# Optimization experiments

Measured on AMD Instinct MI355X. Metric: run time of the kernel, lower is better.

The kernel has to match this reference:

```python
import jax, jax.numpy as jnp
import numpy as np

# Decoder (keras) config: embed_dim=128, num_heads=8, num_att_layers=3, clip=10.0
B, NQ, NC, E, H, L, D = 512, 64, 1000, 128, 8, 3, 4
HD = E // H          # head_depth = 16
CLIP = 10.0


def setup_inputs() -> dict:
    key = jax.random.key(0)
    ks = jax.random.split(key, 12)
    s = 1.0 / np.sqrt(E)

    def w(k, shape):
        return jax.random.normal(k, shape, jnp.float32) * s

    return {
        "h": jax.random.normal(ks[0], (B, NQ, E), jnp.float32),
        "c": jax.random.normal(ks[1], (B, NC, E), jnp.float32),
        "mask": jnp.zeros((B, NQ, NC + 1), bool),
        "clusters": jnp.zeros((B, D, NC), bool),
        "depot_id": 0,
        # stacked per-layer GAT (multi-head self-attention) params [L, E, E]/[L, E]
        "gat_Wq": w(ks[2], (L, E, E)), "gat_bq": jnp.zeros((L, E), jnp.float32),
        "gat_Wk": w(ks[3], (L, E, E)), "gat_bk": jnp.zeros((L, E), jnp.float32),
        "gat_Wv": w(ks[4], (L, E, E)), "gat_bv": jnp.zeros((L, E), jnp.float32),
        "gat_Wo": w(ks[5], (L, E, E)), "gat_bo": jnp.zeros((L, E), jnp.float32),
        # decoder query/key dense layers (use_bias=True)
        "Wq": w(ks[6], (E, E)), "bq": jnp.zeros((E,), jnp.float32),
        "Wk": w(ks[7], (E, E)), "bk": jnp.zeros((E,), jnp.float32),
    }


def _mha_layer(x, Wq, bq, Wk, bk, Wv, bv, Wo, bo):
    # One Graph_Attention_Module: multi-head self-attention + residual.
    Bx, N, Ex = x.shape
    q = (x @ Wq + bq).reshape(Bx, N, H, HD)
    k = (x @ Wk + bk).reshape(Bx, N, H, HD)
    v = (x @ Wv + bv).reshape(Bx, N, H, HD)
    att = jax.nn.softmax(jnp.einsum('bqhd,bkhd->bhqk', q, k) / np.sqrt(HD), axis=-1)
    o = jnp.einsum('bhqk,bkhd->bqhd', att, v).reshape(Bx, N, Ex)
    return x + o @ Wo + bo


def reference(h, c, mask, clusters, depot_id,
              gat_Wq, gat_bq, gat_Wk, gat_bk, gat_Wv, gat_bv, gat_Wo, gat_bo,
              Wq, bq, Wk, bk):
    # --- MHGAT ---
    x = h
    for i in range(L):  # small fixed layer loop
        x = _mha_layer(x, gat_Wq[i], gat_bq[i], gat_Wk[i], gat_bk[i],
                       gat_Wv[i], gat_bv[i], gat_Wo[i], gat_bo[i])
    query = x @ Wq + bq            # [B, NQ, E]
    key = c @ Wk + bk              # [B, NC, E]
    # tanh-clipped compatibility: tanh(QK^T / sqrt(head_depth)) * clip
    compat = jnp.tanh(jnp.einsum('bqe,bke->bqk', query, key) / np.sqrt(HD)) * CLIP
    compat = jnp.where(mask[:, :, 1:], -jnp.inf, compat)   # drop depot column of mask

    # --- select_cust (vectorized: masked log_softmax + argmax per batch) ---
    compts = jnp.mean(compat, axis=1)          # [B, NC]
    clust = clusters[:, depot_id, :]           # [B, NC]
    tt = jnp.where(clust, -jnp.inf, compts)
    log_p = jax.nn.log_softmax(tt, axis=-1)
    action = jnp.argmax(log_p, axis=-1)[:, None]  # [B, 1]
    return action, compat
```

## Files before the change

### kernel.cpp

```cpp
#include <hip/hip_runtime.h>
#include <math.h>

#define NB   512
#define NQ   64
#define NCC  1000
#define EE   128
#define HH   8
#define HDD  16
#define NL   3
#define DD   4
#define CCH  64
#define XP   136
#define VP   72

typedef __bf16 bf16x8 __attribute__((ext_vector_type(8)));
typedef unsigned short u16x8 __attribute__((ext_vector_type(8)));
typedef unsigned short u16x4 __attribute__((ext_vector_type(4)));
typedef unsigned int   u32x4 __attribute__((ext_vector_type(4)));
typedef float f32x4  __attribute__((ext_vector_type(4)));
typedef float f32x16 __attribute__((ext_vector_type(16)));

__device__ __forceinline__ unsigned short f2bf(float x) {
  union { float f; unsigned u; } v; v.f = x;
  unsigned r = (v.u + 0x7fffu + ((v.u >> 16) & 1u)) >> 16;
  return (unsigned short)r;
}
__device__ __forceinline__ float bf2f(unsigned short h) {
  union { unsigned u; float f; } v; v.u = ((unsigned)h) << 16;
  return v.f;
}
__device__ __forceinline__ bf16x8 ld8(const unsigned short* p) {
  return __builtin_bit_cast(bf16x8, *(const u16x8*)p);
}
__device__ __forceinline__ float tanh10_q(float s) {
  const float e = __expf(s * 0.5f);
  return 10.f - 20.f * __builtin_amdgcn_rcpf(e + 1.f);
}
__device__ __forceinline__ int swz(int row, int cb) {
  return row * 256 + (cb ^ ((row & 7) << 4));
}

__global__ __launch_bounds__(256) void wprep_kernel(
    const float* __restrict__ gWq, const float* __restrict__ gWk,
    const float* __restrict__ gWv, const float* __restrict__ gWo,
    const float* __restrict__ Wq,  const float* __restrict__ Wk,
    unsigned short* __restrict__ gwt_hi, unsigned short* __restrict__ gwt_lo,
    unsigned short* __restrict__ wkf_hi, unsigned short* __restrict__ wkf_lo)
{
  const int idx = blockIdx.x * 256 + threadIdx.x;
  const int m = idx >> 14;
  const int r = idx & 16383;
  const int k = r >> 7, n = r & 127;
  const float* src;
  if (m < 12) {
    const int l = m >> 2, w = m & 3;
    src = (w == 0 ? gWq : w == 1 ? gWk : w == 2 ? gWv : gWo) + l * 16384;
  } else if (m == 12) src = Wq;
  else                src = Wk;
  const float v = src[k * EE + n];
  const unsigned short h  = f2bf(v);
  const unsigned short lo = f2bf(v - bf2f(h));
  if (m < 13) {
    gwt_hi[(size_t)m * 16384 + n * EE + k] = h;
    gwt_lo[(size_t)m * 16384 + n * EE + k] = lo;
  } else {
    const int nt = n >> 4, l15 = n & 15;
    const int k4 = k >> 5, qd = (k >> 3) & 3, j = k & 7;
    const int off = (((nt * 4 + k4) * 64) + qd * 16 + l15) * 8 + j;
    wkf_hi[off] = h;
    wkf_lo[off] = lo;
  }
}

__global__ __launch_bounds__(512, 1) void gat_query_mfma(
    const float* __restrict__ hin,
    const unsigned short* __restrict__ gwt_hi,
    const unsigned short* __restrict__ gwt_lo,
    const float* __restrict__ gbq, const float* __restrict__ gbk,
    const float* __restrict__ gbv, const float* __restrict__ gbo,
    const float* __restrict__ bq,
    unsigned short* __restrict__ qhi, unsigned short* __restrict__ qlo)
{
  __shared__ unsigned short XH[64 * XP], XL[64 * XP];
  __shared__ unsigned short QH[64 * XP], QL[64 * XP];
  __shared__ unsigned short KH[64 * XP], KL[64 * XP];
  __shared__ unsigned short VTH[128 * VP], VTL[128 * VP];

  const int b    = blockIdx.x;
  const int tid  = threadIdx.x;
  const int wid  = tid >> 6;
  const int lane = tid & 63;
  const int l15  = lane & 15;
  const int quad = lane >> 4;
  const int col  = lane & 31;
  const int hi32 = lane >> 5;

  for (int idx = tid; idx < NQ * EE; idx += 512) {
    const float v = hin[(size_t)b * NQ * EE + idx];
    const int r = idx >> 7, c = idx & 127;
    const unsigned short h = f2bf(v);
    XH[r * XP + c] = h;
    XL[r * XP + c] = f2bf(v - bf2f(h));
  }
  __syncthreads();

  const int mt = wid >> 1, nh = wid & 1;
  const int r0 = mt * 16;

  for (int l = 0; l < NL; ++l) {
    {
      bf16x8 axh[4], axl[4];
      #pragma unroll
      for (int k4 = 0; k4 < 4; ++k4) {
        axh[k4] = ld8(&XH[(r0 + l15) * XP + k4 * 32 + quad * 8]);
        axl[k4] = ld8(&XL[(r0 + l15) * XP + k4 * 32 + quad * 8]);
      }
      #pragma unroll
      for (int m = 0; m < 3; ++m) {
        const unsigned short* WH = gwt_hi + (size_t)(l * 4 + m) * 16384;
        const unsigned short* WL = gwt_lo + (size_t)(l * 4 + m) * 16384;
        const float* bias = (m == 0 ? gbq : (m == 1 ? gbk : gbv)) + l * EE;
        #pragma unroll
        for (int ntl = 0; ntl < 4; ++ntl) {
          const int n = (nh * 4 + ntl) * 16 + l15;
          f32x4 acc = (f32x4){0.f, 0.f, 0.f, 0.f};
          #pragma unroll
          for (int k4 = 0; k4 < 4; ++k4) {
            const int k0 = k4 * 32 + quad * 8;
            const bf16x8 bh = ld8(&WH[n * EE + k0]);
            const bf16x8 bl = ld8(&WL[n * EE + k0]);
            acc = __builtin_amdgcn_mfma_f32_16x16x32_bf16(axh[k4], bh, acc, 0, 0, 0);
            acc = __builtin_amdgcn_mfma_f32_16x16x32_bf16(axh[k4], bl, acc, 0, 0, 0);
            acc = __builtin_amdgcn_mfma_f32_16x16x32_bf16(axl[k4], bh, acc, 0, 0, 0);
          }
          const float bv = bias[n];
          if (m == 2) {
            u16x4 hv, lv;
            #pragma unroll
            for (int r = 0; r < 4; ++r) {
              const float v = acc[r] + bv;
              const unsigned short h = f2bf(v);
              hv[r] = h;
              lv[r] = f2bf(v - bf2f(h));
            }
            *(u16x4*)&VTH[n * VP + r0 + quad * 4] = hv;
            *(u16x4*)&VTL[n * VP + r0 + quad * 4] = lv;
          } else {
            unsigned short* DH = m ? KH : QH;
            unsigned short* DL = m ? KL : QL;
            #pragma unroll
            for (int r = 0; r < 4; ++r) {
              const int crow = r0 + quad * 4 + r;
              const float v = acc[r] + bv;
              const unsigned short h = f2bf(v);
              DH[crow * XP + n] = h;
              DL[crow * XP + n] = f2bf(v - bf2f(h));
            }
          }
        }
      }
    }
    __syncthreads();

    {
      const int hwid = wid;
      const int hb = hwid * 16 + hi32 * 8;
      bf16x8 akh[2], akl[2], qbh[2], qbl[2];
      #pragma unroll
      for (int t = 0; t < 2; ++t) {
        akh[t] = ld8(&KH[(t * 32 + col) * XP + hb]);
        akl[t] = ld8(&KL[(t * 32 + col) * XP + hb]);
        qbh[t] = ld8(&QH[(t * 32 + col) * XP + hb]);
        qbl[t] = ld8(&QL[(t * 32 + col) * XP + hb]);
      }

      bf16x8 pah[2][4], pal[2][4];
      #pragma unroll
      for (int qt = 0; qt < 2; ++qt) {
        f32x16 sAcc[2];
        #pragma unroll
        for (int kt = 0; kt < 2; ++kt) {
          #pragma unroll
          for (int i = 0; i < 16; ++i) sAcc[kt][i] = 0.f;
          sAcc[kt] = __builtin_amdgcn_mfma_f32_32x32x16_bf16(akh[kt], qbh[qt], sAcc[kt], 0, 0, 0);
          sAcc[kt] = __builtin_amdgcn_mfma_f32_32x32x16_bf16(akh[kt], qbl[qt], sAcc[kt], 0, 0, 0);
          sAcc[kt] = __builtin_amdgcn_mfma_f32_32x32x16_bf16(akl[kt], qbh[qt], sAcc[kt], 0, 0, 0);
        }
        float p[2][16];
        float mx = -INFINITY;
        #pragma unroll
        for (int kt = 0; kt < 2; ++kt)
          #pragma unroll
          for (int r = 0; r < 16; ++r) {
            p[kt][r] = sAcc[kt][r] * 0.25f;
            mx = fmaxf(mx, p[kt][r]);
          }
        mx = fmaxf(mx, __shfl_xor(mx, 32));
        float sum = 0.f;
        #pragma unroll
        for (int kt = 0; kt < 2; ++kt)
          #pragma unroll
          for (int r = 0; r < 16; ++r) {
            p[kt][r] = exp2f((p[kt][r] - mx) * 1.4426950408889634f);
            sum += p[kt][r];
          }
        sum += __shfl_xor(sum, 32);
        const float inv = 1.f / sum;

        unsigned pkh[2][8], pkl[2][8], swh[2][8], swl[2][8];
        #pragma unroll
        for (int kt = 0; kt < 2; ++kt)
          #pragma unroll
          for (int w = 0; w < 8; ++w) {
            const float v0 = p[kt][w * 2]     * inv;
            const float v1 = p[kt][w * 2 + 1] * inv;
            const unsigned short h0 = f2bf(v0);
            const unsigned short l0 = f2bf(v0 - bf2f(h0));
            const unsigned short h1 = f2bf(v1);
            const unsigned short l1 = f2bf(v1 - bf2f(h1));
            pkh[kt][w] = (unsigned)h0 | ((unsigned)h1 << 16);
            pkl[kt][w] = (unsigned)l0 | ((unsigned)l1 << 16);
            swh[kt][w] = (unsigned)__shfl_xor((int)pkh[kt][w], 32);
            swl[kt][w] = (unsigned)__shfl_xor((int)pkl[kt][w], 32);
          }
        const bool top = (hi32 != 0);
        #pragma unroll
        for (int ks = 0; ks < 4; ++ks) {
          const int kt = ks >> 1, hf = ks & 1;
          u32x4 wh, wl;
          wh[0] = top ? swh[kt][4 * hf + 2] : pkh[kt][4 * hf + 0];
          wh[1] = top ? swh[kt][4 * hf + 3] : pkh[kt][4 * hf + 1];
          wh[2] = top ? pkh[kt][4 * hf + 2] : swh[kt][4 * hf + 0];
          wh[3] = top ? pkh[kt][4 * hf + 3] : swh[kt][4 * hf + 1];
          wl[0] = top ? swl[kt][4 * hf + 2] : pkl[kt][4 * hf + 0];
          wl[1] = top ? swl[kt][4 * hf + 3] : pkl[kt][4 * hf + 1];
          wl[2] = top ? pkl[kt][4 * hf + 2] : swl[kt][4 * hf + 0];
          wl[3] = top ? pkl[kt][4 * hf + 3] : swl[kt][4 * hf + 1];
          pah[qt][ks] = __builtin_bit_cast(bf16x8, wh);
          pal[qt][ks] = __builtin_bit_cast(bf16x8, wl);
        }
      }

      bf16x8 bvh[4], bvl[4];
      const int vrow = hwid * 16 + (col & 15);
      #pragma unroll
      for (int ks = 0; ks < 4; ++ks) {
        bvh[ks] = ld8(&VTH[vrow * VP + ks * 16 + hi32 * 8]);
        bvl[ks] = ld8(&VTL[vrow * VP + ks * 16 + hi32 * 8]);
      }
      f32x16 accO[2];
      #pragma unroll
      for (int qt = 0; qt < 2; ++qt) {
        #pragma unroll
        for (int i = 0; i < 16; ++i) accO[qt][i] = 0.f;
        #pragma unroll
        for (int ks = 0; ks < 4; ++ks) {
          accO[qt] = __builtin_amdgcn_mfma_f32_32x32x16_bf16(pah[qt][ks], bvh[ks], accO[qt], 0, 0, 0);
          accO[qt] = __builtin_amdgcn_mfma_f32_32x32x16_bf16(pah[qt][ks], bvl[ks], accO[qt], 0, 0, 0);
          accO[qt] = __builtin_amdgcn_mfma_f32_32x32x16_bf16(pal[qt][ks], bvh[ks], accO[qt], 0, 0, 0);
        }
      }
      if (col < 16) {
        #pragma unroll
        for (int qt = 0; qt < 2; ++qt)
          #pragma unroll
          for (int r = 0; r < 16; ++r) {
            const int qrow = qt * 32 + (r & 3) + 8 * (r >> 2) + 4 * hi32;
            const float v = accO[qt][r];
            const unsigned short h = f2bf(v);
            KH[qrow * XP + hwid * 16 + col] = h;
            KL[qrow * XP + hwid * 16 + col] = f2bf(v - bf2f(h));
          }
      }
    }
    __syncthreads();

    {
      bf16x8 aoh[4], aol[4];
      #pragma unroll
      for (int k4 = 0; k4 < 4; ++k4) {
        aoh[k4] = ld8(&KH[(r0 + l15) * XP + k4 * 32 + quad * 8]);
        aol[k4] = ld8(&KL[(r0 + l15) * XP + k4 * 32 + quad * 8]);
      }
      const unsigned short* WH = gwt_hi + (size_t)(l * 4 + 3) * 16384;
      const unsigned short* WL = gwt_lo + (size_t)(l * 4 + 3) * 16384;
      #pragma unroll
      for (int ntl = 0; ntl < 4; ++ntl) {
        const int n = (nh * 4 + ntl) * 16 + l15;
        f32x4 acc = (f32x4){0.f, 0.f, 0.f, 0.f};
        #pragma unroll
        for (int k4 = 0; k4 < 4; ++k4) {
          const int k0 = k4 * 32 + quad * 8;
          const bf16x8 bh = ld8(&WH[n * EE + k0]);
          const bf16x8 bl = ld8(&WL[n * EE + k0]);
          acc = __builtin_amdgcn_mfma_f32_16x16x32_bf16(aoh[k4], bh, acc, 0, 0, 0);
          acc = __builtin_amdgcn_mfma_f32_16x16x32_bf16(aoh[k4], bl, acc, 0, 0, 0);
          acc = __builtin_amdgcn_mfma_f32_16x16x32_bf16(aol[k4], bh, acc, 0, 0, 0);
        }
        const float bv = gbo[l * EE + n];
        #pragma unroll
        for (int r = 0; r < 4; ++r) {
          const int crow = r0 + quad * 4 + r;
          const float xo = bf2f(XH[crow * XP + n]) + bf2f(XL[crow * XP + n]);
          const float v = xo + acc[r] + bv;
          const unsigned short h = f2bf(v);
          XH[crow * XP + n] = h;
          XL[crow * XP + n] = f2bf(v - bf2f(h));
        }
      }
    }
    __syncthreads();
  }

  {
    bf16x8 axh[4], axl[4];
    #pragma unroll
    for (int k4 = 0; k4 < 4; ++k4) {
      axh[k4] = ld8(&XH[(r0 + l15) * XP + k4 * 32 + quad * 8]);
      axl[k4] = ld8(&XL[(r0 + l15) * XP + k4 * 32 + quad * 8]);
    }
    const unsigned short* WH = gwt_hi + (size_t)12 * 16384;
    const unsigned short* WL = gwt_lo + (size_t)12 * 16384;
    #pragma unroll
    for (int ntl = 0; ntl < 4; ++ntl) {
      const int n = (nh * 4 + ntl) * 16 + l15;
      f32x4 acc = (f32x4){0.f, 0.f, 0.f, 0.f};
      #pragma unroll
      for (int k4 = 0; k4 < 4; ++k4) {
        const int k0 = k4 * 32 + quad * 8;
        const bf16x8 bh = ld8(&WH[n * EE + k0]);
        const bf16x8 bl = ld8(&WL[n * EE + k0]);
        acc = __builtin_amdgcn_mfma_f32_16x16x32_bf16(axh[k4], bh, acc, 0, 0, 0);
        acc = __builtin_amdgcn_mfma_f32_16x16x32_bf16(axh[k4], bl, acc, 0, 0, 0);
        acc = __builtin_amdgcn_mfma_f32_16x16x32_bf16(axl[k4], bh, acc, 0, 0, 0);
      }
      const float bv = bq[n];
      #pragma unroll
      for (int r = 0; r < 4; ++r) {
        const int crow = r0 + quad * 4 + r;
        const float v = acc[r] + bv;
        const unsigned short h = f2bf(v);
        QH[crow * XP + n] = h;
        QL[crow * XP + n] = f2bf(v - bf2f(h));
      }
    }
  }
  __syncthreads();

  for (int it = 0; it < 4; ++it) {
    const int idx  = it * 512 + tid;
    const int part = idx >> 10;
    const int id2  = idx & 1023;
    const int wc   = id2 >> 8;
    const int k4   = (id2 >> 6) & 3;
    const int ln   = id2 & 63;
    const int row  = wc * 16 + (ln & 15);
    const int colu = k4 * 32 + (ln >> 4) * 8;
    const unsigned short* S = part ? QL : QH;
    const u16x8 v = *(const u16x8*)&S[row * XP + colu];
    unsigned short* D = part ? qlo : qhi;
    *(u16x8*)&D[((((size_t)b * 4 + wc) * 4 + k4) * 64 + ln) * 8] = v;
  }
}

__global__ __launch_bounds__(256, 4) void compat_mfma_kernel(
    const float* __restrict__ cin,
    const unsigned short* __restrict__ qhi,
    const unsigned short* __restrict__ qlo,
    const unsigned char* __restrict__ mask,
    const unsigned short* __restrict__ wkf_hi,
    const unsigned short* __restrict__ wkf_lo,
    const float* __restrict__ bk,
    float* __restrict__ compat_out,
    float* __restrict__ compts)
{
  __shared__ unsigned short TH[64 * 128];
  __shared__ unsigned short TL[64 * 128];
  __shared__ float colsum[CCH];

  const int ch   = blockIdx.x;
  const int b    = blockIdx.y;
  const int tid  = threadIdx.x;
  const int wave = tid >> 6;
  const int lane = tid & 63;
  const int l15  = lane & 15;
  const int quad = lane >> 4;

  if (tid < CCH) colsum[tid] = 0.f;

  #pragma unroll
  for (int it = 0; it < 8; ++it) {
    const int lin = it * 256 + tid;
    const int row = lin >> 5;
    const int c16 = lin & 31;
    int grow = ch * CCH + row;
    if (grow > NCC - 1) grow = NCC - 1;
    const float4 x = *(const float4*)&cin[((size_t)b * NCC + grow) * EE + c16 * 4];
    const float xv[4] = {x.x, x.y, x.z, x.w};
    u16x4 h, l;
    #pragma unroll
    for (int j = 0; j < 4; ++j) {
      const unsigned short hb = f2bf(xv[j]);
      h[j] = hb;
      l[j] = f2bf(xv[j] - bf2f(hb));
    }
    const int byt = swz(row, c16 * 8);
    *(u16x4*)((char*)TH + byt) = h;
    *(u16x4*)((char*)TL + byt) = l;
  }
  __syncthreads();

  {
    bf16x8 ahi[4], alo[4];
    const int arow = wave * 16 + l15;
    #pragma unroll
    for (int k4 = 0; k4 < 4; ++k4) {
      const int byt = swz(arow, k4 * 64 + quad * 16);
      ahi[k4] = *(const bf16x8*)((char*)TH + byt);
      alo[k4] = *(const bf16x8*)((char*)TL + byt);
    }
    #pragma unroll
    for (int nt = 0; nt < 8; ++nt) {
      const int n = nt * 16 + l15;
      f32x4 acc = (f32x4){0.f, 0.f, 0.f, 0.f};
      #pragma unroll
      for (int k4 = 0; k4 < 4; ++k4) {
        const size_t foff = (size_t)((nt * 4 + k4) * 64 + lane) * 8;
        const bf16x8 bh = ld8(&wkf_hi[foff]);
        const bf16x8 bl = ld8(&wkf_lo[foff]);
        acc = __builtin_amdgcn_mfma_f32_16x16x32_bf16(ahi[k4], bh, acc, 0, 0, 0);
        acc = __builtin_amdgcn_mfma_f32_16x16x32_bf16(ahi[k4], bl, acc, 0, 0, 0);
        acc = __builtin_amdgcn_mfma_f32_16x16x32_bf16(alo[k4], bh, acc, 0, 0, 0);
      }
      const float bkv = bk[n];
      #pragma unroll
      for (int r = 0; r < 4; ++r) {
        const int crow = wave * 16 + quad * 4 + r;
        const float v = acc[r] + bkv;
        const unsigned short hb = f2bf(v);
        const int byt = swz(crow, n * 2);
        *(unsigned short*)((char*)TH + byt) = hb;
        *(unsigned short*)((char*)TL + byt) = f2bf(v - bf2f(hb));
      }
    }
  }
  __syncthreads();

  {
    bf16x8 qh[4], ql[4];
    #pragma unroll
    for (int k4 = 0; k4 < 4; ++k4) {
      const size_t qoff = ((((size_t)b * 4 + wave) * 4 + k4) * 64 + lane) * 8;
      qh[k4] = ld8(&qhi[qoff]);
      ql[k4] = ld8(&qlo[qoff]);
    }

    f32x4 acc[4];
    #pragma unroll
    for (int nt = 0; nt < 4; ++nt) acc[nt] = (f32x4){0.f, 0.f, 0.f, 0.f};

    #pragma unroll
    for (int k4 = 0; k4 < 4; ++k4) {
      #pragma unroll
      for (int nt = 0; nt < 4; ++nt) {
        const int krow = nt * 16 + l15;
        const int byt = swz(krow, k4 * 64 + quad * 16);
        const bf16x8 khf = *(const bf16x8*)((char*)TH + byt);
        const bf16x8 klf = *(const bf16x8*)((char*)TL + byt);
        acc[nt] = __builtin_amdgcn_mfma_f32_16x16x32_bf16(qh[k4], khf, acc[nt], 0, 0, 0);
        acc[nt] = __builtin_amdgcn_mfma_f32_16x16x32_bf16(qh[k4], klf, acc[nt], 0, 0, 0);
        acc[nt] = __builtin_amdgcn_mfma_f32_16x16x32_bf16(ql[k4], khf, acc[nt], 0, 0, 0);
      }
    }

    #pragma unroll
    for (int nt = 0; nt < 4; ++nt) {
      const int jloc  = nt * 16 + l15;
      const int jglob = ch * CCH + jloc;
      const bool jok  = (jglob < NCC);
      float s4 = 0.f;
      #pragma unroll
      for (int r = 0; r < 4; ++r) {
        const int q = wave * 16 + quad * 4 + r;
        float v = tanh10_q(acc[nt][r]);
        if (jok) {
          if (mask[((size_t)b * NQ + q) * (NCC + 1) + 1 + jglob]) v = -INFINITY;
          compat_out[((size_t)b * NQ + q) * NCC + jglob] = v;
        }
        s4 += v;
      }
      s4 += __shfl_xor(s4, 16);
      s4 += __shfl_xor(s4, 32);
      if (lane < 16 && jok) atomicAdd(&colsum[jloc], s4);
    }
  }
  __syncthreads();

  if (tid < CCH) {
    const int jglob = ch * CCH + tid;
    if (jglob < NCC)
      compts[(size_t)b * 1024 + jglob] = colsum[tid] * (1.0f / (float)NQ);
  }
}

__global__ __launch_bounds__(256) void argmax_kernel(
    const float* __restrict__ compts,
    const unsigned char* __restrict__ clusters,
    const int* __restrict__ depot_id,
    float* __restrict__ out)
{
  __shared__ float redv[256];
  __shared__ int   redi[256];
  const int b   = blockIdx.x;
  const int tid = threadIdx.x;
  const int dep = depot_id[0];
  float bestv = -INFINITY;
  int   besti = 0x7fffffff;
  for (int j = tid; j < NCC; j += 256) {
    float t = compts[(size_t)b * 1024 + j];
    if (clusters[((size_t)b * DD + dep) * NCC + j]) t = -INFINITY;
    if (t > bestv || (t == bestv && j < besti)) { bestv = t; besti = j; }
  }
  redv[tid] = bestv; redi[tid] = besti;
  __syncthreads();
  if (tid == 0) {
    float bv = redv[0]; int bi = redi[0];
    for (int t = 1; t < 256; ++t) {
      if (redv[t] > bv || (redv[t] == bv && redi[t] < bi)) {
        bv = redv[t]; bi = redi[t];
      }
    }
    out[b] = (float)bi;
  }
}

extern "C" void kernel_launch(void* const* d_in, const int* in_sizes, int n_in,
                              void* d_out, int out_size, void* d_ws, size_t ws_size,
                              hipStream_t stream) {
  const float* hin      = (const float*)d_in[0];
  const float* cin      = (const float*)d_in[1];
  const unsigned char* mask     = (const unsigned char*)d_in[2];
  const unsigned char* clusters = (const unsigned char*)d_in[3];
  const int*   depot    = (const int*)d_in[4];
  const float* gWq = (const float*)d_in[5];
  const float* gbq = (const float*)d_in[6];
  const float* gWk = (const float*)d_in[7];
  const float* gbk = (const float*)d_in[8];
  const float* gWv = (const float*)d_in[9];
  const float* gbv = (const float*)d_in[10];
  const float* gWo = (const float*)d_in[11];
  const float* gbo = (const float*)d_in[12];
  const float* Wq  = (const float*)d_in[13];
  const float* bq  = (const float*)d_in[14];
  const float* Wk  = (const float*)d_in[15];
  const float* bk  = (const float*)d_in[16];
  float* out   = (float*)d_out;
  float* compat_out = out + NB;

  unsigned short* qhi    = (unsigned short*)d_ws;
  unsigned short* qlo    = qhi + (size_t)NB * 4 * 4 * 64 * 8;
  float*          compts = (float*)(qlo + (size_t)NB * 4 * 4 * 64 * 8);
  unsigned short* gwt_hi = (unsigned short*)((char*)compts + (size_t)NB * 1024 * 4);
  unsigned short* gwt_lo = gwt_hi + (size_t)14 * 16384;
  unsigned short* wkf_hi = gwt_lo + (size_t)14 * 16384;
  unsigned short* wkf_lo = wkf_hi + (size_t)16384;

  wprep_kernel<<<896, 256, 0, stream>>>(gWq, gWk, gWv, gWo, Wq, Wk,
                                        gwt_hi, gwt_lo, wkf_hi, wkf_lo);
  gat_query_mfma<<<NB, 512, 0, stream>>>(hin, gwt_hi, gwt_lo,
                                         gbq, gbk, gbv, gbo, bq, qhi, qlo);
  compat_mfma_kernel<<<dim3(16, NB), 256, 0, stream>>>(
      cin, qhi, qlo, mask, wkf_hi, wkf_lo, bk, compat_out, compts);
  argmax_kernel<<<NB, 256, 0, stream>>>(compts, clusters, depot, out);
}
```

Before: 828.5 us.

## Restructure GAT kernel per-head to shrink LDS and raise occupancy

Each wave now owns one attention head and computes that head's Q/K/V projection columns for all 64 rows, keeping the results in registers. Those results are staged one at a time through a single shared scratch buffer instead of separate Q/K/V tiles, which cuts LDS use and allows launch bounds of 4 blocks per CU instead of 1. All weights are pre-packed into an MFMA fragment layout so B-operand loads are contiguous per lane. In exchange there is more register pressure (12 accumulators per wave), an extra barrier per layer, and possible register spilling under the tighter launch bound.

Measured after the change: 777.7 us. 6.1% less time.

```diff
diff --git a/kernel.cpp b/kernel.cpp
--- a/kernel.cpp
+++ b/kernel.cpp
@@ -12,6 +12,7 @@
 #define CCH  64
 #define XP   136
 #define VP   72
+#define SCRN 9216
 
 typedef __bf16 bf16x8 __attribute__((ext_vector_type(8)));
 typedef unsigned short u16x8 __attribute__((ext_vector_type(8)));
@@ -44,8 +45,7 @@
     const float* __restrict__ gWq, const float* __restrict__ gWk,
     const float* __restrict__ gWv, const float* __restrict__ gWo,
     const float* __restrict__ Wq,  const float* __restrict__ Wk,
-    unsigned short* __restrict__ gwt_hi, unsigned short* __restrict__ gwt_lo,
-    unsigned short* __restrict__ wkf_hi, unsigned short* __restrict__ wkf_lo)
+    unsigned short* __restrict__ gwf_hi, unsigned short* __restrict__ gwf_lo)
 {
   const int idx = blockIdx.x * 256 + threadIdx.x;
   const int m = idx >> 14;
@@ -60,31 +60,24 @@
   const float v = src[k * EE + n];
   const unsigned short h  = f2bf(v);
   const unsigned short lo = f2bf(v - bf2f(h));
-  if (m < 13) {
-    gwt_hi[(size_t)m * 16384 + n * EE + k] = h;
-    gwt_lo[(size_t)m * 16384 + n * EE + k] = lo;
-  } else {
-    const int nt = n >> 4, l15 = n & 15;
-    const int k4 = k >> 5, qd = (k >> 3) & 3, j = k & 7;
-    const int off = (((nt * 4 + k4) * 64) + qd * 16 + l15) * 8 + j;
-    wkf_hi[off] = h;
-    wkf_lo[off] = lo;
-  }
-}
-
-__global__ __launch_bounds__(512, 1) void gat_query_mfma(
+  const int nt = n >> 4, l15 = n & 15;
+  const int k4 = k >> 5, qd = (k >> 3) & 3, j = k & 7;
+  const size_t off = (size_t)m * 16384 + (((nt * 4 + k4) * 64) + qd * 16 + l15) * 8 + j;
+  gwf_hi[off] = h;
+  gwf_lo[off] = lo;
+}
+
+__global__ __launch_bounds__(512, 4) void gat_query_mfma(
     const float* __restrict__ hin,
-    const unsigned short* __restrict__ gwt_hi,
-    const unsigned short* __restrict__ gwt_lo,
+    const unsigned short* __restrict__ gwf_hi,
+    const unsigned short* __restrict__ gwf_lo,
     const float* __restrict__ gbq, const float* __restrict__ gbk,
     const float* __restrict__ gbv, const float* __restrict__ gbo,
     const float* __restrict__ bq,
     unsigned short* __restrict__ qhi, unsigned short* __restrict__ qlo)
 {
   __shared__ unsigned short XH[64 * XP], XL[64 * XP];
-  __shared__ unsigned short QH[64 * XP], QL[64 * XP];
-  __shared__ unsigned short KH[64 * XP], KL[64 * XP];
-  __shared__ unsigned short VTH[128 * VP], VTL[128 * VP];
+  __shared__ unsigned short SH[SCRN],    SL[SCRN];
 
   const int b    = blockIdx.x;
   const int tid  = threadIdx.x;
@@ -94,184 +87,206 @@
   const int quad = lane >> 4;
   const int col  = lane & 31;
   const int hi32 = lane >> 5;
+  const int h    = wid;
+  const int r0p3 = (wid >> 1) * 16;
+  const int nh   = wid & 1;
 
   for (int idx = tid; idx < NQ * EE; idx += 512) {
     const float v = hin[(size_t)b * NQ * EE + idx];
     const int r = idx >> 7, c = idx & 127;
-    const unsigned short h = f2bf(v);
-    XH[r * XP + c] = h;
-    XL[r * XP + c] = f2bf(v - bf2f(h));
+    const unsigned short hh = f2bf(v);
+    XH[r * XP + c] = hh;
+    XL[r * XP + c] = f2bf(v - bf2f(hh));
   }
   __syncthreads();
 
-  const int mt = wid >> 1, nh = wid & 1;
-  const int r0 = mt * 16;
-
   for (int l = 0; l < NL; ++l) {
+    f32x4 creg[3][4];
+    #pragma unroll
+    for (int mt = 0; mt < 4; ++mt) {
+      bf16x8 axh[4], axl[4];
+      #pragma unroll
+      for (int k4 = 0; k4 < 4; ++k4) {
+        axh[k4] = ld8(&XH[(mt * 16 + l15) * XP + k4 * 32 + quad * 8]);
+        axl[k4] = ld8(&XL[(mt * 16 + l15) * XP + k4 * 32 + quad * 8]);
+      }
+      #pragma unroll
+      for (int m = 0; m < 3; ++m) {
+        const unsigned short* WH = gwf_hi + (size_t)(l * 4 + m) * 16384;
+        const unsigned short* WL = gwf_lo + (size_t)(l * 4 + m) * 16384;
+        f32x4 acc = (f32x4){0.f, 0.f, 0.f, 0.f};
+        #pragma unroll
+        for (int k4 = 0; k4 < 4; ++k4) {
+          const size_t foff = (size_t)((h * 4 + k4) * 64 + lane) * 8;
+          const bf16x8 bh = ld8(&WH[foff]);
+          const bf16x8 bl = ld8(&WL[foff]);
+          acc = __builtin_amdgcn_mfma_f32_16x16x32_bf16(axh[k4], bh, acc, 0, 0, 0);
+          acc = __builtin_amdgcn_mfma_f32_16x16x32_bf16(axh[k4], bl, acc, 0, 0, 0);
+          acc = __builtin_amdgcn_mfma_f32_16x16x32_bf16(axl[k4], bh, acc, 0, 0, 0);
+        }
+        creg[m][mt] = acc;
+      }
+    }
+
     {
-      bf16x8 axh[4], axl[4];
-      #pragma unroll
-      for (int k4 = 0; k4 < 4; ++k4) {
-        axh[k4] = ld8(&XH[(r0 + l15) * XP + k4 * 32 + quad * 8]);
-        axl[k4] = ld8(&XL[(r0 + l15) * XP + k4 * 32 + quad * 8]);
-      }
-      #pragma unroll
-      for (int m = 0; m < 3; ++m) {
-        const unsigned short* WH = gwt_hi + (size_t)(l * 4 + m) * 16384;
-        const unsigned short* WL = gwt_lo + (size_t)(l * 4 + m) * 16384;
-        const float* bias = (m == 0 ? gbq : (m == 1 ? gbk : gbv)) + l * EE;
-        #pragma unroll
-        for (int ntl = 0; ntl < 4; ++ntl) {
-          const int n = (nh * 4 + ntl) * 16 + l15;
-          f32x4 acc = (f32x4){0.f, 0.f, 0.f, 0.f};
-          #pragma unroll
-          for (int k4 = 0; k4 < 4; ++k4) {
-            const int k0 = k4 * 32 + quad * 8;
-            const bf16x8 bh = ld8(&WH[n * EE + k0]);
-            const bf16x8 bl = ld8(&WL[n * EE + k0]);
-            acc = __builtin_amdgcn_mfma_f32_16x16x32_bf16(axh[k4], bh, acc, 0, 0, 0);
-            acc = __builtin_amdgcn_mfma_f32_16x16x32_bf16(axh[k4], bl, acc, 0, 0, 0);
-            acc = __builtin_amdgcn_mfma_f32_16x16x32_bf16(axl[k4], bh, acc, 0, 0, 0);
-          }
-          const float bv = bias[n];
-          if (m == 2) {
-            u16x4 hv, lv;
-            #pragma unroll
-            for (int r = 0; r < 4; ++r) {
-              const float v = acc[r] + bv;
-              const unsigned short h = f2bf(v);
-              hv[r] = h;
-              lv[r] = f2bf(v - bf2f(h));
-            }
-            *(u16x4*)&VTH[n * VP + r0 + quad * 4] = hv;
-            *(u16x4*)&VTL[n * VP + r0 + quad * 4] = lv;
-          } else {
-            unsigned short* DH = m ? KH : QH;
-            unsigned short* DL = m ? KL : QL;
-            #pragma unroll
-            for (int r = 0; r < 4; ++r) {
-              const int crow = r0 + quad * 4 + r;
-              const float v = acc[r] + bv;
-              const unsigned short h = f2bf(v);
-              DH[crow * XP + n] = h;
-              DL[crow * XP + n] = f2bf(v - bf2f(h));
-            }
-          }
-        }
+      const float bv = gbq[l * EE + h * 16 + l15];
+      #pragma unroll
+      for (int mt = 0; mt < 4; ++mt)
+        #pragma unroll
+        for (int r = 0; r < 4; ++r) {
+          const float v = creg[0][mt][r] + bv;
+          const unsigned short hh = f2bf(v);
+          const int o = (mt * 16 + quad * 4 + r) * XP + h * 16 + l15;
+          SH[o] = hh;
+          SL[o] = f2bf(v - bf2f(hh));
+        }
+    }
+    bf16x8 qbh[2], qbl[2];
+    #pragma unroll
+    for (int t = 0; t < 2; ++t) {
+      qbh[t] = ld8(&SH[(t * 32 + col) * XP + h * 16 + hi32 * 8]);
+      qbl[t] = ld8(&SL[(t * 32 + col) * XP + h * 16 + hi32 * 8]);
+    }
+
+    {
+      const float bv = gbk[l * EE + h * 16 + l15];
+      #pragma unroll
+      for (int mt = 0; mt < 4; ++mt)
+        #pragma unroll
+        for (int r = 0; r < 4; ++r) {
+          const float v = creg[1][mt][r] + bv;
+          const unsigned short hh = f2bf(v);
+          const int o = (mt * 16 + quad * 4 + r) * XP + h * 16 + l15;
+          SH[o] = hh;
+          SL[o] = f2bf(v - bf2f(hh));
+        }
+    }
+    bf16x8 akh[2], akl[2];
+    #pragma unroll
+    for (int t = 0; t < 2; ++t) {
+      akh[t] = ld8(&SH[(t * 32 + col) * XP + h * 16 + hi32 * 8]);
+      akl[t] = ld8(&SL[(t * 32 + col) * XP + h * 16 + hi32 * 8]);
+    }
+
+    bf16x8 pah[2][4], pal[2][4];
+    #pragma unroll
+    for (int qt = 0; qt < 2; ++qt) {
+      f32x16 sAcc[2];
+      #pragma unroll
+      for (int kt = 0; kt < 2; ++kt) {
+        #pragma unroll
+        for (int i = 0; i < 16; ++i) sAcc[kt][i] = 0.f;
+        sAcc[kt] = __builtin_amdgcn_mfma_f32_32x32x16_bf16(akh[kt], qbh[qt], sAcc[kt], 0, 0, 0);
+        sAcc[kt] = __builtin_amdgcn_mfma_f32_32x32x16_bf16(akh[kt], qbl[qt], sAcc[kt], 0, 0, 0);
+        sAcc[kt] = __builtin_amdgcn_mfma_f32_32x32x16_bf16(akl[kt], qbh[qt], sAcc[kt], 0, 0, 0);
+      }
+      float p[2][16];
+      float mx = -INFINITY;
+      #pragma unroll
+      for (int kt = 0; kt < 2; ++kt)
+        #pragma unroll
+        for (int r = 0; r < 16; ++r) {
+          p[kt][r] = sAcc[kt][r] * 0.25f;
+          mx = fmaxf(mx, p[kt][r]);
+        }
+      mx = fmaxf(mx, __shfl_xor(mx, 32));
+      float sum = 0.f;
+      #pragma unroll
+      for (int kt = 0; kt < 2; ++kt)
+        #pragma unroll
+        for (int r = 0; r < 16; ++r) {
+          p[kt][r] = exp2f((p[kt][r] - mx) * 1.4426950408889634f);
+          sum += p[kt][r];
+        }
+      sum += __shfl_xor(sum, 32);
+      const float inv = 1.f / sum;
+
+      unsigned pkh[2][8], pkl[2][8], swh[2][8], swl[2][8];
+      #pragma unroll
+      for (int kt = 0; kt < 2; ++kt)
+        #pragma unroll
+        for (int w = 0; w < 8; ++w) {
+          const float v0 = p[kt][w * 2]     * inv;
+          const float v1 = p[kt][w * 2 + 1] * inv;
+          const unsigned short h0 = f2bf(v0);
+          const unsigned short l0 = f2bf(v0 - bf2f(h0));
+          const unsigned short h1 = f2bf(v1);
+          const unsigned short l1 = f2bf(v1 - bf2f(h1));
+          pkh[kt][w] = (unsigned)h0 | ((unsigned)h1 << 16);
+          pkl[kt][w] = (unsigned)l0 | ((unsigned)l1 << 16);
+          swh[kt][w] = (unsigned)__shfl_xor((int)pkh[kt][w], 32);
+          swl[kt][w] = (unsigned)__shfl_xor((int)pkl[kt][w], 32);
+        }
+      const bool top = (hi32 != 0);
+      #pragma unroll
+      for (int ks = 0; ks < 4; ++ks) {
+        const int kt = ks >> 1, hf = ks & 1;
+        u32x4 wh, wl;
+        wh[0] = top ? swh[kt][4 * hf + 2] : pkh[kt][4 * hf + 0];
+        wh[1] = top ? swh[kt][4 * hf + 3] : pkh[kt][4 * hf + 1];
+        wh[2] = top ? pkh[kt][4 * hf + 2] : swh[kt][4 * hf + 0];
+        wh[3] = top ? pkh[kt][4 * hf + 3] : swh[kt][4 * hf + 1];
+        wl[0] = top ? swl[kt][4 * hf + 2] : pkl[kt][4 * hf + 0];
+        wl[1] = top ? swl[kt][4 * hf + 3] : pkl[kt][4 * hf + 1];
+        wl[2] = top ? pkl[kt][4 * hf + 2] : swl[kt][4 * hf + 0];
+        wl[3] = top ? pkl[kt][4 * hf + 3] : swl[kt][4 * hf + 1];
+        pah[qt][ks] = __builtin_bit_cast(bf16x8, wh);
+        pal[qt][ks] = __builtin_bit_cast(bf16x8, wl);
       }
     }
     __syncthreads();
 
     {
-      const int hwid = wid;
-      const int hb = hwid * 16 + hi32 * 8;
-      bf16x8 akh[2], akl[2], qbh[2], qbl[2];
-      #pragma unroll
-      for (int t = 0; t < 2; ++t) {
-        akh[t] = ld8(&KH[(t * 32 + col) * XP + hb]);
-        akl[t] = ld8(&KL[(t * 32 + col) * XP + hb]);
-        qbh[t] = ld8(&QH[(t * 32 + col) * XP + hb]);
-        qbl[t] = ld8(&QL[(t * 32 + col) * XP + hb]);
-      }
-
-      bf16x8 pah[2][4], pal[2][4];
-      #pragma unroll
-      for (int qt = 0; qt < 2; ++qt) {
-        f32x16 sAcc[2];
-        #pragma unroll
-        for (int kt = 0; kt < 2; ++kt) {
-          #pragma unroll
-          for (int i = 0; i < 16; ++i) sAcc[kt][i] = 0.f;
-          sAcc[kt] = __builtin_amdgcn_mfma_f32_32x32x16_bf16(akh[kt], qbh[qt], sAcc[kt], 0, 0, 0);
-          sAcc[kt] = __builtin_amdgcn_mfma_f32_32x32x16_bf16(akh[kt], qbl[qt], sAcc[kt], 0, 0, 0);
-          sAcc[kt] = __builtin_amdgcn_mfma_f32_32x32x16_bf16(akl[kt], qbh[qt], sAcc[kt], 0, 0, 0);
-        }
-        float p[2][16];
-        float mx = -INFINITY;
-        #pragma unroll
-        for (int kt = 0; kt < 2; ++kt)
-          #pragma unroll
-          for (int r = 0; r < 16; ++r) {
-            p[kt][r] = sAcc[kt][r] * 0.25f;
-            mx = fmaxf(mx, p[kt][r]);
-          }
-        mx = fmaxf(mx, __shfl_xor(mx, 32));
-        float sum = 0.f;
-        #pragma unroll
-        for (int kt = 0; kt < 2; ++kt)
-          #pragma unroll
-          for (int r = 0; r < 16; ++r) {
-            p[kt][r] = exp2f((p[kt][r] - mx) * 1.4426950408889634f);
-            sum += p[kt][r];
-          }
-        sum += __shfl_xor(sum, 32);
-        const float inv = 1.f / sum;
-
-        unsigned pkh[2][8], pkl[2][8], swh[2][8], swl[2][8];
-        #pragma unroll
-        for (int kt = 0; kt < 2; ++kt)
-          #pragma unroll
-          for (int w = 0; w < 8; ++w) {
-            const float v0 = p[kt][w * 2]     * inv;
-            const float v1 = p[kt][w * 2 + 1] * inv;
-            const unsigned short h0 = f2bf(v0);
-            const unsigned short l0 = f2bf(v0 - bf2f(h0));
-            const unsigned short h1 = f2bf(v1);
-            const unsigned short l1 = f2bf(v1 - bf2f(h1));
-            pkh[kt][w] = (unsigned)h0 | ((unsigned)h1 << 16);
-            pkl[kt][w] = (unsigned)l0 | ((unsigned)l1 << 16);
-            swh[kt][w] = (unsigned)__shfl_xor((int)pkh[kt][w], 32);
-            swl[kt][w] = (unsigned)__shfl_xor((int)pkl[kt][w], 32);
-          }
-        const bool top = (hi32 != 0);
-        #pragma unroll
-        for (int ks = 0; ks < 4; ++ks) {
-          const int kt = ks >> 1, hf = ks & 1;
-          u32x4 wh, wl;
-          wh[0] = top ? swh[kt][4 * hf + 2] : pkh[kt][4 * hf + 0];
-          wh[1] = top ? swh[kt][4 * hf + 3] : pkh[kt][4 * hf + 1];
-          wh[2] = top ? pkh[kt][4 * hf + 2] : swh[kt][4 * hf + 0];
-          wh[3] = top ? pkh[kt][4 * hf + 3] : swh[kt][4 * hf + 1];
-          wl[0] = top ? swl[kt][4 * hf + 2] : pkl[kt][4 * hf + 0];
-          wl[1] = top ? swl[kt][4 * hf + 3] : pkl[kt][4 * hf + 1];
-          wl[2] = top ? pkl[kt][4 * hf + 2] : swl[kt][4 * hf + 0];
-          wl[3] = top ? pkl[kt][4 * hf + 3] : swl[kt][4 * hf + 1];
-          pah[qt][ks] = __builtin_bit_cast(bf16x8, wh);
-          pal[qt][ks] = __builtin_bit_cast(bf16x8, wl);
-        }
-      }
-
-      bf16x8 bvh[4], bvl[4];
-      const int vrow = hwid * 16 + (col & 15);
+      const float bv = gbv[l * EE + h * 16 + l15];
+      #pragma unroll
+      for (int mt = 0; mt < 4; ++mt) {
+        u16x4 hv, lv;
+        #pragma unroll
+        for (int r = 0; r < 4; ++r) {
+          const float v = creg[2][mt][r] + bv;
+          const unsigned short hh = f2bf(v);
+          hv[r] = hh;
+          lv[r] = f2bf(v - bf2f(hh));
+        }
+        *(u16x4*)&SH[(h * 16 + l15) * VP + mt * 16 + quad * 4] = hv;
+        *(u16x4*)&SL[(h * 16 + l15) * VP + mt * 16 + quad * 4] = lv;
+      }
+    }
+    bf16x8 bvh[4], bvl[4];
+    {
+      const int vrow = h * 16 + (col & 15);
       #pragma unroll
       for (int ks = 0; ks < 4; ++ks) {
-        bvh[ks] = ld8(&VTH[vrow * VP + ks * 16 + hi32 * 8]);
-        bvl[ks] = ld8(&VTL[vrow * VP + ks * 16 + hi32 * 8]);
-      }
-      f32x16 accO[2];
-      #pragma unroll
-      for (int qt = 0; qt < 2; ++qt) {
-        #pragma unroll
-        for (int i = 0; i < 16; ++i) accO[qt][i] = 0.f;
-        #pragma unroll
-        for (int ks = 0; ks < 4; ++ks) {
-          accO[qt] = __builtin_amdgcn_mfma_f32_32x32x16_bf16(pah[qt][ks], bvh[ks], accO[qt], 0, 0, 0);
-          accO[qt] = __builtin_amdgcn_mfma_f32_32x32x16_bf16(pah[qt][ks], bvl[ks], accO[qt], 0, 0, 0);
-          accO[qt] = __builtin_amdgcn_mfma_f32_32x32x16_bf16(pal[qt][ks], bvh[ks], accO[qt], 0, 0, 0);
-        }
-      }
-      if (col < 16) {
-        #pragma unroll
-        for (int qt = 0; qt < 2; ++qt)
-          #pragma unroll
-          for (int r = 0; r < 16; ++r) {
-            const int qrow = qt * 32 + (r & 3) + 8 * (r >> 2) + 4 * hi32;
-            const float v = accO[qt][r];
-            const unsigned short h = f2bf(v);
-            KH[qrow * XP + hwid * 16 + col] = h;
-            KL[qrow * XP + hwid * 16 + col] = f2bf(v - bf2f(h));
-          }
-      }
+        bvh[ks] = ld8(&SH[vrow * VP + ks * 16 + hi32 * 8]);
+        bvl[ks] = ld8(&SL[vrow * VP + ks * 16 + hi32 * 8]);
+      }
+    }
+
+    f32x16 accO[2];
+    #pragma unroll
+    for (int qt = 0; qt < 2; ++qt) {
+      #pragma unroll
+      for (int i = 0; i < 16; ++i) accO[qt][i] = 0.f;
+      #pragma unroll
+      for (int ks = 0; ks < 4; ++ks) {
+        accO[qt] = __builtin_amdgcn_mfma_f32_32x32x16_bf16(pah[qt][ks], bvh[ks], accO[qt], 0, 0, 0);
+        accO[qt] = __builtin_amdgcn_mfma_f32_32x32x16_bf16(pah[qt][ks], bvl[ks], accO[qt], 0, 0, 0);
+        accO[qt] = __builtin_amdgcn_mfma_f32_32x32x16_bf16(pal[qt][ks], bvh[ks], accO[qt], 0, 0, 0);
+      }
+    }
+    __syncthreads();
+
+    if (col < 16) {
+      #pragma unroll
+      for (int qt = 0; qt < 2; ++qt)
+        #pragma unroll
+        for (int r = 0; r < 16; ++r) {
+          const int qrow = qt * 32 + (r & 3) + 8 * (r >> 2) + 4 * hi32;
+          const float v = accO[qt][r];
+          const unsigned short hh = f2bf(v);
+          SH[qrow * XP + h * 16 + col] = hh;
+          SL[qrow * XP + h * 16 + col] = f2bf(v - bf2f(hh));
+        }
     }
     __syncthreads();
 
@@ -279,20 +294,20 @@
       bf16x8 aoh[4], aol[4];
       #pragma unroll
       for (int k4 = 0; k4 < 4; ++k4) {
-        aoh[k4] = ld8(&KH[(r0 + l15) * XP + k4 * 32 + quad * 8]);
-        aol[k4] = ld8(&KL[(r0 + l15) * XP + k4 * 32 + quad * 8]);
-      }
-      const unsigned short* WH = gwt_hi + (size_t)(l * 4 + 3) * 16384;
-      const unsigned short* WL = gwt_lo + (size_t)(l * 4 + 3) * 16384;
+        aoh[k4] = ld8(&SH[(r0p3 + l15) * XP + k4 * 32 + quad * 8]);
+        aol[k4] = ld8(&SL[(r0p3 + l15) * XP + k4 * 32 + quad * 8]);
+      }
+      const unsigned short* WH = gwf_hi + (size_t)(l * 4 + 3) * 16384;
+      const unsigned short* WL = gwf_lo + (size_t)(l * 4 + 3) * 16384;
       #pragma unroll
       for (int ntl = 0; ntl < 4; ++ntl) {
         const int n = (nh * 4 + ntl) * 16 + l15;
         f32x4 acc = (f32x4){0.f, 0.f, 0.f, 0.f};
         #pragma unroll
         for (int k4 = 0; k4 < 4; ++k4) {
-          const int k0 = k4 * 32 + quad * 8;
-          const bf16x8 bh = ld8(&WH[n * EE + k0]);
-          const bf16x8 bl = ld8(&WL[n * EE + k0]);
+          const size_t foff = (size_t)(((nh * 4 + ntl) * 4 + k4) * 64 + lane) * 8;
+          const bf16x8 bh = ld8(&WH[foff]);
+          const bf16x8 bl = ld8(&WL[foff]);
           acc = __builtin_amdgcn_mfma_f32_16x16x32_bf16(aoh[k4], bh, acc, 0, 0, 0);
           acc = __builtin_amdgcn_mfma_f32_16x16x32_bf16(aoh[k4], bl, acc, 0, 0, 0);
           acc = __builtin_amdgcn_mfma_f32_16x16x32_bf16(aol[k4], bh, acc, 0, 0, 0);
@@ -300,12 +315,12 @@
         const float bv = gbo[l * EE + n];
         #pragma unroll
         for (int r = 0; r < 4; ++r) {
-          const int crow = r0 + quad * 4 + r;
+          const int crow = r0p3 + quad * 4 + r;
           const float xo = bf2f(XH[crow * XP + n]) + bf2f(XL[crow * XP + n]);
           const float v = xo + acc[r] + bv;
-          const unsigned short h = f2bf(v);
-          XH[crow * XP + n] = h;
-          XL[crow * XP + n] = f2bf(v - bf2f(h));
+          const unsigned short hh = f2bf(v);
+          XH[crow * XP + n] = hh;
+          XL[crow * XP + n] = f2bf(v - bf2f(hh));
         }
       }
     }
@@ -313,35 +328,34 @@
   }
 
   {
-    bf16x8 axh[4], axl[4];
-    #pragma unroll
-    for (int k4 = 0; k4 < 4; ++k4) {
-      axh[k4] = ld8(&XH[(r0 + l15) * XP + k4 * 32 + quad * 8]);
-      axl[k4] = ld8(&XL[(r0 + l15) * XP + k4 * 32 + quad * 8]);
-    }
-    const unsigned short* WH = gwt_hi + (size_t)12 * 16384;
-    const unsigned short* WL = gwt_lo + (size_t)12 * 16384;
-    #pragma unroll
-    for (int ntl = 0; ntl < 4; ++ntl) {
-      const int n = (nh * 4 + ntl) * 16 + l15;
+    const unsigned short* WH = gwf_hi + (size_t)12 * 16384;
+    const unsigned short* WL = gwf_lo + (size_t)12 * 16384;
+    const float bv = bq[h * 16 + l15];
+    #pragma unroll
+    for (int mt = 0; mt < 4; ++mt) {
+      bf16x8 axh[4], axl[4];
+      #pragma unroll
+      for (int k4 = 0; k4 < 4; ++k4) {
+        axh[k4] = ld8(&XH[(mt * 16 + l15) * XP + k4 * 32 + quad * 8]);
+        axl[k4] = ld8(&XL[(mt * 16 + l15) * XP + k4 * 32 + quad * 8]);
+      }
       f32x4 acc = (f32x4){0.f, 0.f, 0.f, 0.f};
       #pragma unroll
       for (int k4 = 0; k4 < 4; ++k4) {
-        const int k0 = k4 * 32 + quad * 8;
-        const bf16x8 bh = ld8(&WH[n * EE + k0]);
-        const bf16x8 bl = ld8(&WL[n * EE + k0]);
+        const size_t foff = (size_t)((h * 4 + k4) * 64 + lane) * 8;
+        const bf16x8 bh = ld8(&WH[foff]);
+        const bf16x8 bl = ld8(&WL[foff]);
         acc = __builtin_amdgcn_mfma_f32_16x16x32_bf16(axh[k4], bh, acc, 0, 0, 0);
         acc = __builtin_amdgcn_mfma_f32_16x16x32_bf16(axh[k4], bl, acc, 0, 0, 0);
         acc = __builtin_amdgcn_mfma_f32_16x16x32_bf16(axl[k4], bh, acc, 0, 0, 0);
       }
-      const float bv = bq[n];
       #pragma unroll
       for (int r = 0; r < 4; ++r) {
-        const int crow = r0 + quad * 4 + r;
         const float v = acc[r] + bv;
-        const unsigned short h = f2bf(v);
-        QH[crow * XP + n] = h;
-        QL[crow * XP + n] = f2bf(v - bf2f(h));
+        const unsigned short hh = f2bf(v);
+        const int o = (mt * 16 + quad * 4 + r) * XP + h * 16 + l15;
+        SH[o] = hh;
+        SL[o] = f2bf(v - bf2f(hh));
       }
     }
   }
@@ -356,7 +370,7 @@
     const int ln   = id2 & 63;
     const int row  = wc * 16 + (ln & 15);
     const int colu = k4 * 32 + (ln >> 4) * 8;
-    const unsigned short* S = part ? QL : QH;
+    const unsigned short* S = part ? SL : SH;
     const u16x8 v = *(const u16x8*)&S[row * XP + colu];
     unsigned short* D = part ? qlo : qhi;
     *(u16x8*)&D[((((size_t)b * 4 + wc) * 4 + k4) * 64 + ln) * 8] = v;
@@ -560,14 +574,14 @@
   unsigned short* qhi    = (unsigned short*)d_ws;
   unsigned short* qlo    = qhi + (size_t)NB * 4 * 4 * 64 * 8;
   float*          compts = (float*)(qlo + (size_t)NB * 4 * 4 * 64 * 8);
-  unsigned short* gwt_hi = (unsigned short*)((char*)compts + (size_t)NB * 1024 * 4);
-  unsigned short* gwt_lo = gwt_hi + (size_t)14 * 16384;
-  unsigned short* wkf_hi = gwt_lo + (size_t)14 * 16384;
-  unsigned short* wkf_lo = wkf_hi + (size_t)16384;
+  unsigned short* gwf_hi = (unsigned short*)((char*)compts + (size_t)NB * 1024 * 4);
+  unsigned short* gwf_lo = gwf_hi + (size_t)14 * 16384;
+  unsigned short* wkf_hi = gwf_hi + (size_t)13 * 16384;
+  unsigned short* wkf_lo = gwf_lo + (size_t)13 * 16384;
 
   wprep_kernel<<<896, 256, 0, stream>>>(gWq, gWk, gWv, gWo, Wq, Wk,
-                                        gwt_hi, gwt_lo, wkf_hi, wkf_lo);
-  gat_query_mfma<<<NB, 512, 0, stream>>>(hin, gwt_hi, gwt_lo,
+                                        gwf_hi, gwf_lo);
+  gat_query_mfma<<<NB, 512, 0, stream>>>(hin, gwf_hi, gwf_lo,
                                          gbq, gbk, gbv, gbo, bq, qhi, qlo);
   compat_mfma_kernel<<<dim3(16, NB), 256, 0, stream>>>(
       cin, qhi, qlo, mask, wkf_hi, wkf_lo, bk, compat_out, compts);
```
